# Optimization experiments

Hardware: AMD Instinct MI355X
Metric: run time of the kernel (lower is better)

Reference implementation:

```python
import jax, jax.numpy as jnp
import numpy as np

K = 7          # kernel_size
G = 16         # group_number
C = 256        # channel
R = 4          # reduction_ratio
BN_EPS = 1e-3  # keras BatchNormalization default epsilon


def setup_inputs() -> dict:
    key = jax.random.key(0)
    ks = jax.random.split(key, 8)
    B, H, W = 2, 64, 64
    Cr = C // R
    x = jax.random.normal(ks[0], (B, H, W, C), dtype=jnp.float32)
    # kernel_gen params: 1x1 conv (C->C/r), BN, ReLU, 1x1 conv (C/r -> K*K*G)
    w1 = jax.random.normal(ks[1], (C, Cr), dtype=jnp.float32) * (1.0 / np.sqrt(C))
    b1 = jnp.zeros((Cr,), dtype=jnp.float32)
    gamma = jnp.ones((Cr,), dtype=jnp.float32) + 0.1 * jax.random.normal(ks[2], (Cr,), dtype=jnp.float32)
    beta = 0.1 * jax.random.normal(ks[3], (Cr,), dtype=jnp.float32)
    mu = 0.1 * jax.random.normal(ks[4], (Cr,), dtype=jnp.float32)
    var = jnp.ones((Cr,), dtype=jnp.float32) + 0.05 * jax.random.uniform(ks[5], (Cr,), dtype=jnp.float32)
    w2 = jax.random.normal(ks[6], (Cr, K * K * G), dtype=jnp.float32) * (1.0 / np.sqrt(Cr))
    b2 = jnp.zeros((K * K * G,), dtype=jnp.float32)
    return {"x": x, "w1": w1, "b1": b1, "gamma": gamma, "beta": beta,
            "mu": mu, "var": var, "w2": w2, "b2": b2}


def reference(x, w1, b1, gamma, beta, mu, var, w2, b2):
    B, H, W, _ = x.shape
    # stride == 1 -> stride_layer is identity; kernel_input = x
    # kernel_gen: 1x1 conv -> BN (inference) -> ReLU -> 1x1 conv
    t = jnp.einsum('bhwc,cd->bhwd', x, w1) + b1
    t = gamma * (t - mu) * jax.lax.rsqrt(var + BN_EPS) + beta
    t = jax.nn.relu(t)
    kern = jnp.einsum('bhwd,dk->bhwk', t, w2) + b2            # (B,H,W,K*K*G)
    kern = kern.reshape(B, H, W, K * K, 1, G)                  # (B,H,W,KK,1,G)
    # tf.image.extract_patches SAME, stride 1 -> pad K//2 each side, zeros
    pad = K // 2
    xp = jnp.pad(x, ((0, 0), (pad, pad), (pad, pad), (0, 0)))
    # patch layout matches TF: (kh, kw) outer, channel inner
    patches = jnp.stack(
        [xp[:, i:i + H, j:j + W, :] for i in range(K) for j in range(K)],
        axis=3)                                                # (B,H,W,KK,C)
    patches = patches.reshape(B, H, W, K * K, C // G, G)
    out = jnp.sum(kern * patches, axis=3)                      # (B,H,W,C/G,G)
    out = out.reshape(B, H, W, C)
    return out, kern
```

## Files before the change

### kernel.cpp

```cpp
#include <hip/hip_runtime.h>


typedef __attribute__((ext_vector_type(8))) short short8;
typedef __attribute__((ext_vector_type(4))) float f32x4;

#define OUT_ELEMS 2097152
#define W2S_OFF 0
#define W1S_OFF 131072
#define BNS_OFF (131072 + 32768)
#define BNH_OFF (BNS_OFF + 256)

static __device__ __forceinline__ ushort f2bf(float f) {
    union { float f; unsigned u; } v; v.f = f;
    return (ushort)((v.u + 0x7FFFu + ((v.u >> 16) & 1u)) >> 16);
}

__global__ __launch_bounds__(256)
void prep(const float* __restrict__ w1, const float* __restrict__ w2,
          const float* __restrict__ b1, const float* __restrict__ gamma_,
          const float* __restrict__ beta_, const float* __restrict__ mu_,
          const float* __restrict__ var_, char* __restrict__ base)
{
    const int g = blockIdx.x * 256 + threadIdx.x;
    ushort* w2s = (ushort*)(base + W2S_OFF);
    ushort* w1s = (ushort*)(base + W1S_OFF);
    float*  bns = (float*)(base + BNS_OFF);
    float*  bnh = (float*)(base + BNH_OFF);
    if (g < 50176) {
        const int e = g & 7, lane = (g >> 3) & 63, kgks = g >> 9;
        const int kg = kgks >> 1, ks = kgks & 1;
        const int n = kg * 16 + (lane & 15);
        const int k = ks * 32 + ((lane >> 4) << 3) + e;
        w2s[g] = f2bf(w2[k * 784 + n]);
    } else if (g < 66560) {
        const int e2 = g - 50176;
        const int e = e2 & 7, lane = (e2 >> 3) & 63, ntks = e2 >> 9;
        const int nt = ntks >> 3, ks = ntks & 7;
        const int n = nt * 16 + (lane & 15);
        const int k = ks * 32 + ((lane >> 4) << 3) + e;
        w1s[e2] = f2bf(w1[k * 64 + n]);
    } else if (g < 66624) {
        const int d = g - 66560;
        const float s = gamma_[d] * rsqrtf(var_[d] + 1e-3f);
        bns[d] = s;
        bnh[d] = beta_[d] + (b1[d] - mu_[d]) * s;
    }
}

#define FMA4(A, K, X) \
    A.x = fmaf(K.x, X.x, A.x); A.y = fmaf(K.y, X.y, A.y); \
    A.z = fmaf(K.z, X.z, A.z); A.w = fmaf(K.w, X.w, A.w);

__global__ __launch_bounds__(256)
void invol_fused(const float* __restrict__ x, const char* __restrict__ base,
                 const float* __restrict__ b2, float* __restrict__ kern_out,
                 float* __restrict__ out)
{
    __shared__ __align__(16) union {
        struct { ushort xb[4096]; ushort tb[1024]; } s;
        float kl[12544];
    } u;

    const ushort* w2s = (const ushort*)(base + W2S_OFF);
    const ushort* w1s = (const ushort*)(base + W1S_OFF);
    const float*  bns = (const float*)(base + BNS_OFF);
    const float*  bnh = (const float*)(base + BNH_OFF);

    const int tid  = threadIdx.x;
    const int lane = tid & 63;
    const int wv   = tid >> 6;
    const int bid  = blockIdx.x;
    const int pb   = ((bid & 7) << 10) + ((bid >> 3) << 4);
    const int b  = pb >> 12;
    const int h  = (pb >> 6) & 63;
    const int w0 = pb & 63;

#pragma unroll
    for (int i = 0; i < 4; ++i) {
        const int f4 = tid + 256 * i;
        const int px = f4 >> 6;
        const int c0 = (f4 & 63) * 4;
        const float4 v = *(const float4*)(x + (size_t)(pb + px) * 256 + c0);
        ushort4 hh;
        hh.x = f2bf(v.x); hh.y = f2bf(v.y); hh.z = f2bf(v.z); hh.w = f2bf(v.w);
        const int byte = ((px << 9) + (c0 << 1)) ^ ((px & 7) << 4);
        *(ushort4*)((char*)u.s.xb + byte) = hh;
    }
    __syncthreads();

    const int qlane = lane >> 4;
    const int mrow  = lane & 15;
    const int aswz  = (mrow & 7) << 4;

    f32x4 acc = {0.f, 0.f, 0.f, 0.f};
#pragma unroll
    for (int ks = 0; ks < 8; ++ks) {
        const short8 a = *(const short8*)((const char*)u.s.xb +
                          (((mrow << 9) + ((ks * 32 + qlane * 8) << 1)) ^ aswz));
        const short8 bv = *(const short8*)(w1s + ((wv * 8 + ks) * 64 + lane) * 8);
        acc = __builtin_amdgcn_mfma_f32_16x16x32_bf16(a, bv, acc, 0, 0, 0);
    }
    {
        const int col = wv * 16 + mrow;
        const float s = bns[col], sh = bnh[col];
#pragma unroll
        for (int r = 0; r < 4; ++r) {
            const int row = qlane * 4 + r;
            const float tv = fmaxf(fmaf(acc[r], s, sh), 0.f);
            const int byte = ((row << 7) + (col << 1)) ^ ((row & 7) << 4);
            *(ushort*)((char*)u.s.tb + byte) = f2bf(tv);
        }
    }
    __syncthreads();

    const short8 a0 = *(const short8*)((const char*)u.s.tb +
                        (((mrow << 7) + (qlane << 4)) ^ aswz));
    const short8 a1 = *(const short8*)((const char*)u.s.tb +
                        (((mrow << 7) + 64 + (qlane << 4)) ^ aswz));
    __syncthreads();

    for (int kg = wv; kg < 49; kg += 4) {
        const short8 bv0 = *(const short8*)(w2s + (size_t)((kg * 2 + 0) * 64 + lane) * 8);
        const short8 bv1 = *(const short8*)(w2s + (size_t)((kg * 2 + 1) * 64 + lane) * 8);
        f32x4 c = {0.f, 0.f, 0.f, 0.f};
        c = __builtin_amdgcn_mfma_f32_16x16x32_bf16(a0, bv0, c, 0, 0, 0);
        c = __builtin_amdgcn_mfma_f32_16x16x32_bf16(a1, bv1, c, 0, 0, 0);
        const int n = kg * 16 + mrow;
        const float bias = b2[n];
#pragma unroll
        for (int r = 0; r < 4; ++r) {
            const int row = qlane * 4 + r;
            const float val = c[r] + bias;
            kern_out[(size_t)(pb + row) * 784 + n] = val;
            u.kl[row * 784 + n] = val;
        }
    }
    __syncthreads();

    const int c0  = lane * 4;
    const int g0  = c0 & 15;
    const int w0w = w0 + wv * 4;
    const float* xbase = x + ((size_t)b << 20);

    float msk[10]; int colc[10];
#pragma unroll
    for (int j = 0; j < 10; ++j) {
        const int cw = w0w + j - 3;
        msk[j]  = ((unsigned)cw < 64u) ? 1.0f : 0.0f;
        colc[j] = (min(max(cw, 0), 63) << 8) + c0;
    }

    float4 acc4[4];
#pragma unroll
    for (int p = 0; p < 4; ++p) acc4[p] = make_float4(0.f, 0.f, 0.f, 0.f);

#pragma unroll
    for (int kh = 0; kh < 7; ++kh) {
        const int hh = h + kh - 3;
        if ((unsigned)hh < 64u) {
            const float* xr = xbase + ((size_t)hh << 14);
            float4 xv[10];
#pragma unroll
            for (int j = 0; j < 10; ++j) {
                xv[j] = *(const float4*)(xr + colc[j]);
                xv[j].x *= msk[j]; xv[j].y *= msk[j];
                xv[j].z *= msk[j]; xv[j].w *= msk[j];
            }
#pragma unroll
            for (int p = 0; p < 4; ++p) {
                const float* kr = u.kl + (wv * 4 + p) * 784 + kh * 112 + g0;
#pragma unroll
                for (int kw = 0; kw < 7; ++kw) {
                    const float4 kv = *(const float4*)(kr + kw * 16);
                    FMA4(acc4[p], kv, xv[p + kw]);
                }
            }
        }
    }
#pragma unroll
    for (int p = 0; p < 4; ++p)
        *(float4*)(out + (size_t)(pb + wv * 4 + p) * 256 + c0) = acc4[p];
}

extern "C" void kernel_launch(void* const* d_in, const int* in_sizes, int n_in,
                              void* d_out, int out_size, void* d_ws, size_t ws_size,
                              hipStream_t stream)
{
    const float* x      = (const float*)d_in[0];
    const float* w1     = (const float*)d_in[1];
    const float* b1     = (const float*)d_in[2];
    const float* gamma_ = (const float*)d_in[3];
    const float* beta_  = (const float*)d_in[4];
    const float* mu_    = (const float*)d_in[5];
    const float* var_   = (const float*)d_in[6];
    const float* w2     = (const float*)d_in[7];
    const float* b2     = (const float*)d_in[8];

    float* out  = (float*)d_out;
    float* kern = out + OUT_ELEMS;
    char*  base = (char*)d_out;

    prep<<<261, 256, 0, stream>>>(w1, w2, b1, gamma_, beta_, mu_, var_, base);
    invol_fused<<<512, 256, 0, stream>>>(x, base, b2, kern, out);
}
```

Measured before the change: 96.23 us.

## Prefetch w2 fragments, split tb from union, make row-boundary loads branchless

Moves the bf16 activation tile out of the shared-memory union so the barrier before the second GEMM can be dropped. The loop software-prefetches w2 weight fragments two iterations ahead to hide global load latency behind the MFMAs. The involution loop replaces the per-row boundary branch with a clamped row index and a zero multiplier, letting all loads issue unconditionally. It also moves the prepared-weight scratch from the output buffer to the workspace, and costs some extra registers and some redundant loads at edge rows.

```diff
diff --git a/kernel.cpp b/kernel.cpp
--- a/kernel.cpp
+++ b/kernel.cpp
@@ -57,9 +57,10 @@
                  float* __restrict__ out)
 {
     __shared__ __align__(16) union {
-        struct { ushort xb[4096]; ushort tb[1024]; } s;
-        float kl[12544];
+        ushort xb[4096];
+        float  kl[12544];
     } u;
+    __shared__ __align__(16) ushort tb[1024];
 
     const ushort* w2s = (const ushort*)(base + W2S_OFF);
     const ushort* w1s = (const ushort*)(base + W1S_OFF);
@@ -84,7 +85,7 @@
         ushort4 hh;
         hh.x = f2bf(v.x); hh.y = f2bf(v.y); hh.z = f2bf(v.z); hh.w = f2bf(v.w);
         const int byte = ((px << 9) + (c0 << 1)) ^ ((px & 7) << 4);
-        *(ushort4*)((char*)u.s.xb + byte) = hh;
+        *(ushort4*)((char*)u.xb + byte) = hh;
     }
     __syncthreads();
 
@@ -95,7 +96,7 @@
     f32x4 acc = {0.f, 0.f, 0.f, 0.f};
 #pragma unroll
     for (int ks = 0; ks < 8; ++ks) {
-        const short8 a = *(const short8*)((const char*)u.s.xb +
+        const short8 a = *(const short8*)((const char*)u.xb +
                           (((mrow << 9) + ((ks * 32 + qlane * 8) << 1)) ^ aswz));
         const short8 bv = *(const short8*)(w1s + ((wv * 8 + ks) * 64 + lane) * 8);
         acc = __builtin_amdgcn_mfma_f32_16x16x32_bf16(a, bv, acc, 0, 0, 0);
@@ -108,23 +109,35 @@
             const int row = qlane * 4 + r;
             const float tv = fmaxf(fmaf(acc[r], s, sh), 0.f);
             const int byte = ((row << 7) + (col << 1)) ^ ((row & 7) << 4);
-            *(ushort*)((char*)u.s.tb + byte) = f2bf(tv);
+            *(ushort*)((char*)tb + byte) = f2bf(tv);
         }
     }
     __syncthreads();
 
-    const short8 a0 = *(const short8*)((const char*)u.s.tb +
+    const short8 a0 = *(const short8*)((const char*)tb +
                         (((mrow << 7) + (qlane << 4)) ^ aswz));
-    const short8 a1 = *(const short8*)((const char*)u.s.tb +
+    const short8 a1 = *(const short8*)((const char*)tb +
                         (((mrow << 7) + 64 + (qlane << 4)) ^ aswz));
-    __syncthreads();
-
+
+    short8 wa0, wa1, wb0, wb1;
+    {
+        wa0 = *(const short8*)(w2s + (size_t)((wv * 2 + 0) * 64 + lane) * 8);
+        wa1 = *(const short8*)(w2s + (size_t)((wv * 2 + 1) * 64 + lane) * 8);
+        const int k1 = (wv + 4 < 49) ? wv + 4 : wv;
+        wb0 = *(const short8*)(w2s + (size_t)((k1 * 2 + 0) * 64 + lane) * 8);
+        wb1 = *(const short8*)(w2s + (size_t)((k1 * 2 + 1) * 64 + lane) * 8);
+    }
+#pragma unroll 2
     for (int kg = wv; kg < 49; kg += 4) {
-        const short8 bv0 = *(const short8*)(w2s + (size_t)((kg * 2 + 0) * 64 + lane) * 8);
-        const short8 bv1 = *(const short8*)(w2s + (size_t)((kg * 2 + 1) * 64 + lane) * 8);
+        const short8 ua = wa0, ub = wa1;
+        wa0 = wb0; wa1 = wb1;
+        const int kn = (kg + 8 < 49) ? kg + 8 : wv;
+        wb0 = *(const short8*)(w2s + (size_t)((kn * 2 + 0) * 64 + lane) * 8);
+        wb1 = *(const short8*)(w2s + (size_t)((kn * 2 + 1) * 64 + lane) * 8);
+
         f32x4 c = {0.f, 0.f, 0.f, 0.f};
-        c = __builtin_amdgcn_mfma_f32_16x16x32_bf16(a0, bv0, c, 0, 0, 0);
-        c = __builtin_amdgcn_mfma_f32_16x16x32_bf16(a1, bv1, c, 0, 0, 0);
+        c = __builtin_amdgcn_mfma_f32_16x16x32_bf16(a0, ua, c, 0, 0, 0);
+        c = __builtin_amdgcn_mfma_f32_16x16x32_bf16(a1, ub, c, 0, 0, 0);
         const int n = kg * 16 + mrow;
         const float bias = b2[n];
 #pragma unroll
@@ -157,23 +170,23 @@
 #pragma unroll
     for (int kh = 0; kh < 7; ++kh) {
         const int hh = h + kh - 3;
-        if ((unsigned)hh < 64u) {
-            const float* xr = xbase + ((size_t)hh << 14);
-            float4 xv[10];
-#pragma unroll
-            for (int j = 0; j < 10; ++j) {
-                xv[j] = *(const float4*)(xr + colc[j]);
-                xv[j].x *= msk[j]; xv[j].y *= msk[j];
-                xv[j].z *= msk[j]; xv[j].w *= msk[j];
-            }
-#pragma unroll
-            for (int p = 0; p < 4; ++p) {
-                const float* kr = u.kl + (wv * 4 + p) * 784 + kh * 112 + g0;
-#pragma unroll
-                for (int kw = 0; kw < 7; ++kw) {
-                    const float4 kv = *(const float4*)(kr + kw * 16);
-                    FMA4(acc4[p], kv, xv[p + kw]);
-                }
+        const float rm = ((unsigned)hh < 64u) ? 1.0f : 0.0f;
+        const int hc = min(max(hh, 0), 63);
+        const float* xr = xbase + ((size_t)hc << 14);
+        float4 xv[10];
+#pragma unroll
+        for (int j = 0; j < 10; ++j) {
+            xv[j] = *(const float4*)(xr + colc[j]);
+            const float s = msk[j] * rm;
+            xv[j].x *= s; xv[j].y *= s; xv[j].z *= s; xv[j].w *= s;
+        }
+#pragma unroll
+        for (int p = 0; p < 4; ++p) {
+            const float* kr = u.kl + (wv * 4 + p) * 784 + kh * 112 + g0;
+#pragma unroll
+            for (int kw = 0; kw < 7; ++kw) {
+                const float4 kv = *(const float4*)(kr + kw * 16);
+                FMA4(acc4[p], kv, xv[p + kw]);
             }
         }
     }
@@ -198,7 +211,7 @@
 
     float* out  = (float*)d_out;
     float* kern = out + OUT_ELEMS;
-    char*  base = (char*)d_out;
+    char*  base = (char*)d_ws;
 
     prep<<<261, 256, 0, stream>>>(w1, w2, b1, gamma_, beta_, mu_, var_, base);
     invol_fused<<<512, 256, 0, stream>>>(x, base, b2, kern, out);
```

New measurement: 97.22 us. No clear change (+1.0%).
